# Kernel optimization log

Measured on AMD Instinct MI355X. Metric: run time of the kernel, lower is better.

Reference implementation:

```python
import jax, jax.numpy as jnp
import numpy as np

B, N, K = 1, 100000, 16
C_IN, C_OUT = 64, 128
C_MID = C_OUT // 4            # unary1 output channels (32)
PE_H = C_OUT // 4             # pe_convs hidden (32)
PE_OUT = min(C_OUT // 4, 32)  # pe_convs output (32)
WN_IN, WN_H, WN_OUT = 3, 8, 16


def _lin(key, i, o):
    return jax.random.normal(key, (i, o), jnp.float32) * (1.0 / np.sqrt(i))


def setup_inputs() -> dict:
    key = jax.random.key(0)
    ks = jax.random.split(key, 13)
    return {
        "dense_xyz": jax.random.normal(ks[0], (B, N, 3), jnp.float32),
        "dense_feats": jax.random.normal(ks[1], (B, N, C_IN), jnp.float32),
        "nei_inds": jax.random.randint(ks[2], (B, N, K), 0, N),
        "pe_w1": _lin(ks[3], 3, PE_H), "pe_b1": jnp.zeros((PE_H,), jnp.float32),
        "pe_w2": _lin(ks[4], PE_H, PE_OUT), "pe_b2": jnp.zeros((PE_OUT,), jnp.float32),
        "u1_w": _lin(ks[5], C_IN, C_MID), "u1_b": jnp.zeros((C_MID,), jnp.float32),
        "wn_w1": _lin(ks[6], WN_IN, WN_H), "wn_b1": jnp.zeros((WN_H,), jnp.float32),
        "wn_w2": _lin(ks[7], WN_H, WN_H), "wn_b2": jnp.zeros((WN_H,), jnp.float32),
        "wn_w3": _lin(ks[8], WN_H, WN_OUT), "wn_b3": jnp.zeros((WN_OUT,), jnp.float32),
        "lin_w": _lin(ks[9], (C_MID + PE_OUT) * WN_OUT, C_OUT // 2),
        "lin_b": jnp.zeros((C_OUT // 2,), jnp.float32),
        "u2_w": _lin(ks[10], C_OUT // 2, C_OUT), "u2_b": jnp.zeros((C_OUT,), jnp.float32),
        "sc_w": _lin(ks[11], C_IN, C_OUT), "sc_b": jnp.zeros((C_OUT,), jnp.float32),
    }


def _act(x):
    # act_layer = LeakyReLU(0.1)
    return jax.nn.leaky_relu(x, 0.1)


def reference(dense_xyz, dense_feats, nei_inds, pe_w1, pe_b1, pe_w2, pe_b2,
              u1_w, u1_b, wn_w1, wn_b1, wn_w2, wn_b2, wn_w3, wn_b3,
              lin_w, lin_b, u2_w, u2_b, sc_w, sc_b):
    gather = jax.vmap(lambda x, i: x[i])  # per-batch fancy gather
    g_xyz = gather(dense_xyz, nei_inds)                 # B,N,K,3
    localized = g_xyz - dense_xyz[:, :, None, :]        # weightNetInput (USE_VI=False)
    # positional-embedding WeightNet: Linear+act, Linear+act
    pe = _act(localized @ pe_w1 + pe_b1)
    pe = _act(pe @ pe_w2 + pe_b2)                       # B,N,K,PE_OUT
    # unary1 bottleneck (no act in PointLinearLayer default)
    feats = dense_feats @ u1_w + u1_b                   # B,N,C_MID
    g_feat = gather(feats, nei_inds)                    # B,N,K,C_MID
    new_feat = jnp.concatenate([g_feat, pe], axis=-1)   # B,N,K,C_MID+PE_OUT
    # WeightNet on localized coords: act, none, act
    w = _act(localized @ wn_w1 + wn_b1)
    w = w @ wn_w2 + wn_b2
    w = _act(w @ wn_w3 + wn_b3)                         # B,N,K,WN_OUT
    # PointConv aggregation: feats^T @ weights over neighbors
    agg = jnp.einsum('bnkc,bnkw->bncw', new_feat, w)
    agg = agg.reshape(agg.shape[0], agg.shape[1], -1)   # B,N,(C_MID+PE_OUT)*WN_OUT
    x = _act(agg @ lin_w + lin_b)                       # linear + act (norm=None)
    x = x @ u2_w + u2_b                                 # unary2, no act
    shortcut = dense_feats @ sc_w + sc_b                # unary_shortcut (in!=out)
    out = _act(x + shortcut)
    return out, localized
```

## Files before the change

### kernel.cpp

```cpp
#include <hip/hip_runtime.h>
#include <stdint.h>

#define NPTS 100000
#define KNEI 16
#define CIN 64
#define CMID 32
#define CONC 64
#define LINI 1024
#define COUT 128
#define APITCH 1032

typedef unsigned short u16;
typedef unsigned int u32;
typedef __attribute__((ext_vector_type(8))) short bf16x8;
typedef __attribute__((ext_vector_type(4))) float f32x4;

#define WS_PACKB  6400000
#define WS_PACKW2 (WS_PACKB + 131072)
#define WS_WN     (WS_PACKW2 + 32768)

#define NB_U1 1563
#define NB_PACK 256
#define NB_PACKW2 64

__device__ __forceinline__ float lrelu(float x) { return x > 0.f ? x : 0.1f * x; }

__device__ __forceinline__ u32 f2bf(float f) {
    union { float f; u32 u; } v; v.f = f;
    return (v.u + 0x7FFFu + ((v.u >> 16) & 1u)) >> 16;
}
__device__ __forceinline__ u16 f2bfF(float f) {
    union { float f; u32 u; } v; v.f = f;
    return (u16)((v.u + 0x8000u) >> 16);
}
__device__ __forceinline__ u32 pkbf(float a, float b) {
    union { float f; u32 u; } x, y; x.f = a; y.f = b;
    return __builtin_amdgcn_perm(y.u + 0x8000u, x.u + 0x8000u, 0x07060302u);
}
__device__ __forceinline__ float bf2f(u32 h) {
    union { u32 u; float f; } v; v.u = h << 16; return v.f;
}

__global__ __launch_bounds__(256) void k_prep(
    const float* __restrict__ df, const float* __restrict__ u1_w,
    const float* __restrict__ u1_b, u32* __restrict__ feats2,
    const float* __restrict__ lin_w, u16* __restrict__ packB,
    const float* __restrict__ u2_w, const float* __restrict__ sc_w,
    u16* __restrict__ packW2,
    const float* __restrict__ wn_w2, const float* __restrict__ wn_b2,
    const float* __restrict__ wn_w3, const float* __restrict__ wn_b3,
    float* __restrict__ wnf)
{
    int bid = blockIdx.x;
    if (bid < NB_U1) {
        const int wv = threadIdx.x >> 6, lane = threadIdx.x & 63;
        const int quad = lane >> 4, nl = lane & 15;
        const int pbase = bid * 64 + wv * 16;
        if (pbase >= NPTS) return;

        bf16x8 bw[2][2];
        #pragma unroll
        for (int nt = 0; nt < 2; ++nt)
            #pragma unroll
            for (int kk = 0; kk < 2; ++kk)
                #pragma unroll
                for (int j = 0; j < 8; ++j)
                    bw[nt][kk][j] = (short)f2bf(u1_w[(kk * 32 + quad * 8 + j) * CMID + nt * 16 + nl]);

        const float* arow = df + (size_t)(pbase + nl) * CIN + quad * 8;
        float4 a0 = *(const float4*)(arow + 0);
        float4 a1 = *(const float4*)(arow + 4);
        float4 a2 = *(const float4*)(arow + 32);
        float4 a3 = *(const float4*)(arow + 36);
        bf16x8 afr0, afr1;
        u32* ap0 = (u32*)&afr0; u32* ap1 = (u32*)&afr1;
        ap0[0] = pkbf(a0.x, a0.y); ap0[1] = pkbf(a0.z, a0.w);
        ap0[2] = pkbf(a1.x, a1.y); ap0[3] = pkbf(a1.z, a1.w);
        ap1[0] = pkbf(a2.x, a2.y); ap1[1] = pkbf(a2.z, a2.w);
        ap1[2] = pkbf(a3.x, a3.y); ap1[3] = pkbf(a3.z, a3.w);

        const f32x4 z = {0.f, 0.f, 0.f, 0.f};
        f32x4 acc0 = z, acc1 = z;
        acc0 = __builtin_amdgcn_mfma_f32_16x16x32_bf16(afr0, bw[0][0], acc0, 0, 0, 0);
        acc0 = __builtin_amdgcn_mfma_f32_16x16x32_bf16(afr1, bw[0][1], acc0, 0, 0, 0);
        acc1 = __builtin_amdgcn_mfma_f32_16x16x32_bf16(afr0, bw[1][0], acc1, 0, 0, 0);
        acc1 = __builtin_amdgcn_mfma_f32_16x16x32_bf16(afr1, bw[1][1], acc1, 0, 0, 0);

        float blo = u1_b[nl], bhi = u1_b[16 + nl];
        #pragma unroll
        for (int r = 0; r < 4; ++r) {
            int pt = pbase + quad * 4 + r;
            feats2[(size_t)pt * 16 + nl] = f2bf(acc0[r] + blo) | (f2bf(acc1[r] + bhi) << 16);
        }
    } else if (bid < NB_U1 + NB_PACK) {
        int t = (bid - NB_U1) * 256 + threadIdx.x;
        int j = t & 7, ln = (t >> 3) & 63, s = t >> 9;
        int nt = s & 3, kb = s >> 2;
        int k = kb * 32 + (ln >> 4) * 8 + j;
        int n = nt * 16 + (ln & 15);
        packB[t] = (u16)f2bf(lin_w[k * 64 + n]);
    } else if (bid < NB_U1 + NB_PACK + NB_PACKW2) {
        int t = (bid - NB_U1 - NB_PACK) * 256 + threadIdx.x;
        int j = t & 7, ln = (t >> 3) & 63, s = t >> 9;
        int nt2 = s & 7, kb2 = s >> 3;
        int k = kb2 * 32 + (ln >> 4) * 8 + j;
        int n = nt2 * 16 + (ln & 15);
        float v = (k < 64) ? u2_w[k * COUT + n] : sc_w[(k - 64) * COUT + n];
        packW2[t] = (u16)f2bf(v);
    } else {
        int t = threadIdx.x;
        if (t < 128) {
            int i = t >> 4, o = t & 15;
            float a = 0.f;
            #pragma unroll
            for (int m = 0; m < 8; ++m) a += wn_w2[i * 8 + m] * wn_w3[m * 16 + o];
            wnf[i * 16 + o] = a;
        } else if (t < 144) {
            int o = t - 128;
            float a = wn_b3[o];
            #pragma unroll
            for (int m = 0; m < 8; ++m) a += wn_b2[m] * wn_w3[m * 16 + o];
            wnf[128 + o] = a;
        }
    }
}

__global__ __launch_bounds__(256) void k_fused(
    const float* __restrict__ xyz, const int* __restrict__ nei,
    const u32* __restrict__ feats2,
    const float* __restrict__ pe_w1, const float* __restrict__ pe_b1,
    const float* __restrict__ pe_w2, const float* __restrict__ pe_b2,
    const float* __restrict__ wn_w1, const float* __restrict__ wn_b1,
    const float* __restrict__ wnf,
    const u16* __restrict__ packB, const u16* __restrict__ packW2,
    const float* __restrict__ lin_b,
    const float* __restrict__ u2_b, const float* __restrict__ sc_b,
    const float* __restrict__ df, float* __restrict__ out,
    float* __restrict__ locout)
{
    __shared__ __align__(16) u16 aggL[16 * APITCH];
    __shared__ float loc_s[4][4][16][3];
    __shared__ int   idx_s[4][4][16];
    __shared__ __align__(16) u16 pexd[4][32][24];
    __shared__ __align__(16) u16 w_s[4][16][24];
    __shared__ __align__(16) u16 h1_s[4][4][16][8];

    u16* xd = &pexd[0][0][0];

    const int tid = threadIdx.x, wv = tid >> 6, lane = tid & 63;
    const int quad = lane >> 4, nl = lane & 15;
    const int p0 = blockIdx.x * 16;
    const int ptBase = p0 + wv * 4;

    int pt0 = ptBase + quad;
    int idx0 = nei[pt0 * KNEI + nl];
    idx_s[wv][quad][nl] = idx0;
    {
        float cx = xyz[pt0 * 3 + 0], cy = xyz[pt0 * 3 + 1], cz = xyz[pt0 * 3 + 2];
        float lx0 = xyz[idx0 * 3 + 0] - cx;
        float ly0 = xyz[idx0 * 3 + 1] - cy;
        float lz0 = xyz[idx0 * 3 + 2] - cz;
        loc_s[wv][quad][nl][0] = lx0;
        loc_s[wv][quad][nl][1] = ly0;
        loc_s[wv][quad][nl][2] = lz0;
        float* lo = locout + (size_t)(pt0 * KNEI + nl) * 3;
        lo[0] = lx0; lo[1] = ly0; lo[2] = lz0;
        uint4 hp;
        u32* hpp = (u32*)&hp;
        #pragma unroll
        for (int h = 0; h < 8; h += 2) {
            float a = lrelu(wn_b1[h]     + lx0 * wn_w1[h]     + ly0 * wn_w1[8 + h]     + lz0 * wn_w1[16 + h]);
            float b = lrelu(wn_b1[h + 1] + lx0 * wn_w1[h + 1] + ly0 * wn_w1[8 + h + 1] + lz0 * wn_w1[16 + h + 1]);
            hpp[h >> 1] = pkbf(a, b);
        }
        *(uint4*)&h1_s[wv][quad][nl][0] = hp;
    }

    float w1r0[8], w1r1[8], w1r2[8], b1v[8];
    #pragma unroll
    for (int j = 0; j < 8; ++j) {
        int h = quad * 8 + j;
        w1r0[j] = pe_w1[h]; w1r1[j] = pe_w1[32 + h]; w1r2[j] = pe_w1[64 + h];
        b1v[j] = pe_b1[h];
    }
    bf16x8 w2t[2];
    #pragma unroll
    for (int ct = 0; ct < 2; ++ct)
        #pragma unroll
        for (int j = 0; j < 8; ++j)
            w2t[ct][j] = (short)f2bf(pe_w2[(quad * 8 + j) * 32 + nl + 16 * ct]);
    float b2v[2][4];
    #pragma unroll
    for (int ct = 0; ct < 2; ++ct)
        #pragma unroll
        for (int r = 0; r < 4; ++r)
            b2v[ct][r] = pe_b2[16 * ct + quad * 4 + r];
    float wn3v[8][4], b23v[4];
    #pragma unroll
    for (int h = 0; h < 8; ++h)
        #pragma unroll
        for (int r = 0; r < 4; ++r)
            wn3v[h][r] = wnf[h * 16 + quad * 4 + r];
    #pragma unroll
    for (int r = 0; r < 4; ++r) b23v[r] = wnf[128 + quad * 4 + r];

    const f32x4 zacc = {0.f, 0.f, 0.f, 0.f};

    for (int p = 0; p < 4; ++p) {
        const int m = wv * 4 + p;

        bf16x8 featf0 = 0, featf1 = 0;
        if (quad < 2) {
            #pragma unroll
            for (int j = 0; j < 8; ++j) {
                int idk = idx_s[wv][p][quad * 8 + j];
                u32 v = feats2[(size_t)idk * 16 + nl];
                featf0[j] = (short)(v & 0xffffu);
                featf1[j] = (short)(v >> 16);
            }
        }

        float lx = loc_s[wv][p][nl][0];
        float ly = loc_s[wv][p][nl][1];
        float lz = loc_s[wv][p][nl][2];

        bf16x8 phf;
        {
            u32* ph32 = (u32*)&phf;
            #pragma unroll
            for (int j = 0; j < 8; j += 2) {
                float v0 = lrelu(b1v[j]     + lx * w1r0[j]     + ly * w1r1[j]     + lz * w1r2[j]);
                float v1 = lrelu(b1v[j + 1] + lx * w1r0[j + 1] + ly * w1r1[j + 1] + lz * w1r2[j + 1]);
                ph32[j >> 1] = pkbf(v0, v1);
            }
        }

        f32x4 pe0 = __builtin_amdgcn_mfma_f32_16x16x32_bf16(w2t[0], phf, zacc, 0, 0, 0);
        f32x4 pe1 = __builtin_amdgcn_mfma_f32_16x16x32_bf16(w2t[1], phf, zacc, 0, 0, 0);

        #pragma unroll
        for (int r = 0; r < 4; ++r) {
            pexd[wv][quad * 4 + r][nl]      = f2bfF(lrelu(pe0[r] + b2v[0][r]));
            pexd[wv][16 + quad * 4 + r][nl] = f2bfF(lrelu(pe1[r] + b2v[1][r]));
        }

        {
            uint4 hv = *(const uint4*)&h1_s[wv][p][nl][0];
            float h1f[8];
            h1f[0] = bf2f(hv.x & 0xffffu); h1f[1] = bf2f(hv.x >> 16);
            h1f[2] = bf2f(hv.y & 0xffffu); h1f[3] = bf2f(hv.y >> 16);
            h1f[4] = bf2f(hv.z & 0xffffu); h1f[5] = bf2f(hv.z >> 16);
            h1f[6] = bf2f(hv.w & 0xffffu); h1f[7] = bf2f(hv.w >> 16);
            #pragma unroll
            for (int r = 0; r < 4; ++r) {
                float a = b23v[r];
                #pragma unroll
                for (int h = 0; h < 8; ++h) a += h1f[h] * wn3v[h][r];
                w_s[wv][quad * 4 + r][nl] = f2bfF(lrelu(a));
            }
        }

        bf16x8 wA = 0, peB0 = 0, peB1 = 0;
        if (quad < 2) {
            wA   = *(const bf16x8*)&w_s[wv][nl][quad * 8];
            peB0 = *(const bf16x8*)&pexd[wv][nl][quad * 8];
            peB1 = *(const bf16x8*)&pexd[wv][nl + 16][quad * 8];
        }

        f32x4 c0a = __builtin_amdgcn_mfma_f32_16x16x32_bf16(wA, featf0, zacc, 0, 0, 0);
        f32x4 c1a = __builtin_amdgcn_mfma_f32_16x16x32_bf16(wA, featf1, zacc, 0, 0, 0);
        f32x4 c2a = __builtin_amdgcn_mfma_f32_16x16x32_bf16(wA, peB0, zacc, 0, 0, 0);
        f32x4 c3a = __builtin_amdgcn_mfma_f32_16x16x32_bf16(wA, peB1, zacc, 0, 0, 0);

        {
            u16* arow = aggL + m * APITCH;
            f32x4 cc[4] = {c0a, c1a, c2a, c3a};
            #pragma unroll
            for (int ct = 0; ct < 4; ++ct) {
                int e = (nl + 16 * ct) * 16 + quad * 4;
                uint2 o;
                o.x = pkbf(cc[ct][0], cc[ct][1]);
                o.y = pkbf(cc[ct][2], cc[ct][3]);
                *(uint2*)(arow + e) = o;
            }
        }
    }
    __syncthreads();

    const int nt = wv;
    {
        const u16* bp = packB + nt * 512 + lane * 8;
        const u16* arow = aggL + nl * APITCH;
        f32x4 accA = zacc, accB = zacc;
        #pragma unroll
        for (int kk = 0; kk < 16; ++kk) {
            int kbA = 2 * kk, kbB = 2 * kk + 1;
            bf16x8 aA = *(const bf16x8*)(arow + (4 * kbA + quad) * 8);
            bf16x8 aB = *(const bf16x8*)(arow + (4 * kbB + quad) * 8);
            bf16x8 bA = *(const bf16x8*)(bp + kbA * 2048);
            bf16x8 bB = *(const bf16x8*)(bp + kbB * 2048);
            accA = __builtin_amdgcn_mfma_f32_16x16x32_bf16(aA, bA, accA, 0, 0, 0);
            accB = __builtin_amdgcn_mfma_f32_16x16x32_bf16(aB, bB, accB, 0, 0, 0);
        }
        int col = nt * 16 + nl;
        float lb = lin_b[col];
        int kb2 = col >> 5, q2 = (col >> 3) & 3, j2 = col & 7;
        #pragma unroll
        for (int r = 0; r < 4; ++r) {
            int mm = quad * 4 + r;
            float v = lrelu(accA[r] + accB[r] + lb);
            xd[(kb2 * 64 + q2 * 16 + mm) * 8 + j2] = f2bfF(v);
        }
    }
    if (tid < 128) {
        int mm = tid >> 3, cg = tid & 7;
        int colk = 64 + cg * 8;
        const float* dfr = df + (size_t)(p0 + mm) * CIN + cg * 8;
        float4 f0 = *(const float4*)(dfr);
        float4 f1 = *(const float4*)(dfr + 4);
        int kb2 = colk >> 5, q2 = (colk >> 3) & 3;
        uint4 o;
        o.x = pkbf(f0.x, f0.y);
        o.y = pkbf(f0.z, f0.w);
        o.z = pkbf(f1.x, f1.y);
        o.w = pkbf(f1.z, f1.w);
        *(uint4*)(xd + (kb2 * 64 + q2 * 16 + mm) * 8) = o;
    }
    __syncthreads();

    {
        f32x4 acc20 = zacc, acc21 = zacc;
        #pragma unroll
        for (int kb = 0; kb < 4; ++kb) {
            bf16x8 a = *(const bf16x8*)(xd + (kb * 64 + lane) * 8);
            bf16x8 b0 = *(const bf16x8*)(packW2 + (size_t)(kb * 8 + wv * 2 + 0) * 512 + lane * 8);
            bf16x8 b1 = *(const bf16x8*)(packW2 + (size_t)(kb * 8 + wv * 2 + 1) * 512 + lane * 8);
            acc20 = __builtin_amdgcn_mfma_f32_16x16x32_bf16(a, b0, acc20, 0, 0, 0);
            acc21 = __builtin_amdgcn_mfma_f32_16x16x32_bf16(a, b1, acc21, 0, 0, 0);
        }
        #pragma unroll
        for (int t = 0; t < 2; ++t) {
            f32x4 ac = t ? acc21 : acc20;
            int colo = (wv * 2 + t) * 16 + nl;
            float bias = u2_b[colo] + sc_b[colo];
            #pragma unroll
            for (int r = 0; r < 4; ++r) {
                int mm = quad * 4 + r;
                out[(size_t)(p0 + mm) * COUT + colo] = lrelu(ac[r] + bias);
            }
        }
    }
}

extern "C" void kernel_launch(void* const* d_in, const int* in_sizes, int n_in,
                              void* d_out, int out_size, void* d_ws, size_t ws_size,
                              hipStream_t stream) {
    const float* xyz   = (const float*)d_in[0];
    const float* df    = (const float*)d_in[1];
    const int*   nei   = (const int*)d_in[2];
    const float* pe_w1 = (const float*)d_in[3];
    const float* pe_b1 = (const float*)d_in[4];
    const float* pe_w2 = (const float*)d_in[5];
    const float* pe_b2 = (const float*)d_in[6];
    const float* u1_w  = (const float*)d_in[7];
    const float* u1_b  = (const float*)d_in[8];
    const float* wn_w1 = (const float*)d_in[9];
    const float* wn_b1 = (const float*)d_in[10];
    const float* wn_w2 = (const float*)d_in[11];
    const float* wn_b2 = (const float*)d_in[12];
    const float* wn_w3 = (const float*)d_in[13];
    const float* wn_b3 = (const float*)d_in[14];
    const float* lin_w = (const float*)d_in[15];
    const float* lin_b = (const float*)d_in[16];
    const float* u2_w  = (const float*)d_in[17];
    const float* u2_b  = (const float*)d_in[18];
    const float* sc_w  = (const float*)d_in[19];
    const float* sc_b  = (const float*)d_in[20];

    u32* feats2 = (u32*)d_ws;
    u16* packB  = (u16*)((char*)d_ws + WS_PACKB);
    u16* packW2 = (u16*)((char*)d_ws + WS_PACKW2);
    float* wnf  = (float*)((char*)d_ws + WS_WN);
    float* outp = (float*)d_out;
    float* locout = outp + (size_t)NPTS * COUT;

    hipLaunchKernelGGL(k_prep, dim3(NB_U1 + NB_PACK + NB_PACKW2 + 1), dim3(256), 0, stream,
                       df, u1_w, u1_b, feats2, lin_w, packB, u2_w, sc_w, packW2,
                       wn_w2, wn_b2, wn_w3, wn_b3, wnf);

    hipLaunchKernelGGL(k_fused, dim3(NPTS / 16), dim3(256), 0, stream,
                       xyz, nei, feats2,
                       pe_w1, pe_b1, pe_w2, pe_b2,
                       wn_w1, wn_b1, wnf,
                       packB, packW2, lin_b, u2_b, sc_b,
                       df, outp, locout);
}
```

Measured before the change: 227.2 us.

## Process two point groups per block and amortize weight setup in prep and fused kernels

The fused kernel now loops over two 16-point groups per block and launches half as many blocks, so per-thread register loads of the small MLP weights are paid once per 32 points. The prep kernel likewise lets each wave handle four 16-point tiles, so the bf16 u1 weight fragments are built once per 64 points instead of once per 16. Smaller tweaks replace the branchy leaky ReLU with fmaxf, unpack gathered features with byte-permute instructions, and write the localized output as a float3 store. The cost is fewer blocks in flight, which can hide less latency, plus an extra block-wide barrier between the two groups.

```diff
diff --git a/kernel.cpp b/kernel.cpp
--- a/kernel.cpp
+++ b/kernel.cpp
@@ -19,11 +19,11 @@
 #define WS_PACKW2 (WS_PACKB + 131072)
 #define WS_WN     (WS_PACKW2 + 32768)
 
-#define NB_U1 1563
+#define NB_U1 391
 #define NB_PACK 256
 #define NB_PACKW2 64
 
-__device__ __forceinline__ float lrelu(float x) { return x > 0.f ? x : 0.1f * x; }
+__device__ __forceinline__ float lrelu(float x) { return fmaxf(x, 0.1f * x); }
 
 __device__ __forceinline__ u32 f2bf(float f) {
     union { float f; u32 u; } v; v.f = f;
@@ -55,8 +55,8 @@
     if (bid < NB_U1) {
         const int wv = threadIdx.x >> 6, lane = threadIdx.x & 63;
         const int quad = lane >> 4, nl = lane & 15;
-        const int pbase = bid * 64 + wv * 16;
-        if (pbase >= NPTS) return;
+        const int base = bid * 256 + wv * 64;
+        if (base >= NPTS) return;
 
         bf16x8 bw[2][2];
         #pragma unroll
@@ -67,30 +67,37 @@
                 for (int j = 0; j < 8; ++j)
                     bw[nt][kk][j] = (short)f2bf(u1_w[(kk * 32 + quad * 8 + j) * CMID + nt * 16 + nl]);
 
-        const float* arow = df + (size_t)(pbase + nl) * CIN + quad * 8;
-        float4 a0 = *(const float4*)(arow + 0);
-        float4 a1 = *(const float4*)(arow + 4);
-        float4 a2 = *(const float4*)(arow + 32);
-        float4 a3 = *(const float4*)(arow + 36);
-        bf16x8 afr0, afr1;
-        u32* ap0 = (u32*)&afr0; u32* ap1 = (u32*)&afr1;
-        ap0[0] = pkbf(a0.x, a0.y); ap0[1] = pkbf(a0.z, a0.w);
-        ap0[2] = pkbf(a1.x, a1.y); ap0[3] = pkbf(a1.z, a1.w);
-        ap1[0] = pkbf(a2.x, a2.y); ap1[1] = pkbf(a2.z, a2.w);
-        ap1[2] = pkbf(a3.x, a3.y); ap1[3] = pkbf(a3.z, a3.w);
-
+        float blo = u1_b[nl], bhi = u1_b[16 + nl];
         const f32x4 z = {0.f, 0.f, 0.f, 0.f};
-        f32x4 acc0 = z, acc1 = z;
-        acc0 = __builtin_amdgcn_mfma_f32_16x16x32_bf16(afr0, bw[0][0], acc0, 0, 0, 0);
-        acc0 = __builtin_amdgcn_mfma_f32_16x16x32_bf16(afr1, bw[0][1], acc0, 0, 0, 0);
-        acc1 = __builtin_amdgcn_mfma_f32_16x16x32_bf16(afr0, bw[1][0], acc1, 0, 0, 0);
-        acc1 = __builtin_amdgcn_mfma_f32_16x16x32_bf16(afr1, bw[1][1], acc1, 0, 0, 0);
-
-        float blo = u1_b[nl], bhi = u1_b[16 + nl];
+
         #pragma unroll
-        for (int r = 0; r < 4; ++r) {
-            int pt = pbase + quad * 4 + r;
-            feats2[(size_t)pt * 16 + nl] = f2bf(acc0[r] + blo) | (f2bf(acc1[r] + bhi) << 16);
+        for (int g = 0; g < 4; ++g) {
+            int pbase = base + g * 16;
+            if (pbase >= NPTS) break;
+
+            const float* arow = df + (size_t)(pbase + nl) * CIN + quad * 8;
+            float4 a0 = *(const float4*)(arow + 0);
+            float4 a1 = *(const float4*)(arow + 4);
+            float4 a2 = *(const float4*)(arow + 32);
+            float4 a3 = *(const float4*)(arow + 36);
+            bf16x8 afr0, afr1;
+            u32* ap0 = (u32*)&afr0; u32* ap1 = (u32*)&afr1;
+            ap0[0] = pkbf(a0.x, a0.y); ap0[1] = pkbf(a0.z, a0.w);
+            ap0[2] = pkbf(a1.x, a1.y); ap0[3] = pkbf(a1.z, a1.w);
+            ap1[0] = pkbf(a2.x, a2.y); ap1[1] = pkbf(a2.z, a2.w);
+            ap1[2] = pkbf(a3.x, a3.y); ap1[3] = pkbf(a3.z, a3.w);
+
+            f32x4 acc0 = z, acc1 = z;
+            acc0 = __builtin_amdgcn_mfma_f32_16x16x32_bf16(afr0, bw[0][0], acc0, 0, 0, 0);
+            acc0 = __builtin_amdgcn_mfma_f32_16x16x32_bf16(afr1, bw[0][1], acc0, 0, 0, 0);
+            acc1 = __builtin_amdgcn_mfma_f32_16x16x32_bf16(afr0, bw[1][0], acc1, 0, 0, 0);
+            acc1 = __builtin_amdgcn_mfma_f32_16x16x32_bf16(afr1, bw[1][1], acc1, 0, 0, 0);
+
+            #pragma unroll
+            for (int r = 0; r < 4; ++r) {
+                int pt = pbase + quad * 4 + r;
+                feats2[(size_t)pt * 16 + nl] = f2bf(acc0[r] + blo) | (f2bf(acc1[r] + bhi) << 16);
+            }
         }
     } else if (bid < NB_U1 + NB_PACK) {
         int t = (bid - NB_U1) * 256 + threadIdx.x;
@@ -149,32 +156,6 @@
 
     const int tid = threadIdx.x, wv = tid >> 6, lane = tid & 63;
     const int quad = lane >> 4, nl = lane & 15;
-    const int p0 = blockIdx.x * 16;
-    const int ptBase = p0 + wv * 4;
-
-    int pt0 = ptBase + quad;
-    int idx0 = nei[pt0 * KNEI + nl];
-    idx_s[wv][quad][nl] = idx0;
-    {
-        float cx = xyz[pt0 * 3 + 0], cy = xyz[pt0 * 3 + 1], cz = xyz[pt0 * 3 + 2];
-        float lx0 = xyz[idx0 * 3 + 0] - cx;
-        float ly0 = xyz[idx0 * 3 + 1] - cy;
-        float lz0 = xyz[idx0 * 3 + 2] - cz;
-        loc_s[wv][quad][nl][0] = lx0;
-        loc_s[wv][quad][nl][1] = ly0;
-        loc_s[wv][quad][nl][2] = lz0;
-        float* lo = locout + (size_t)(pt0 * KNEI + nl) * 3;
-        lo[0] = lx0; lo[1] = ly0; lo[2] = lz0;
-        uint4 hp;
-        u32* hpp = (u32*)&hp;
-        #pragma unroll
-        for (int h = 0; h < 8; h += 2) {
-            float a = lrelu(wn_b1[h]     + lx0 * wn_w1[h]     + ly0 * wn_w1[8 + h]     + lz0 * wn_w1[16 + h]);
-            float b = lrelu(wn_b1[h + 1] + lx0 * wn_w1[h + 1] + ly0 * wn_w1[8 + h + 1] + lz0 * wn_w1[16 + h + 1]);
-            hpp[h >> 1] = pkbf(a, b);
-        }
-        *(uint4*)&h1_s[wv][quad][nl][0] = hp;
-    }
 
     float w1r0[8], w1r1[8], w1r2[8], b1v[8];
     #pragma unroll
@@ -206,147 +187,183 @@
 
     const f32x4 zacc = {0.f, 0.f, 0.f, 0.f};
 
-    for (int p = 0; p < 4; ++p) {
-        const int m = wv * 4 + p;
-
-        bf16x8 featf0 = 0, featf1 = 0;
-        if (quad < 2) {
-            #pragma unroll
-            for (int j = 0; j < 8; ++j) {
-                int idk = idx_s[wv][p][quad * 8 + j];
-                u32 v = feats2[(size_t)idk * 16 + nl];
-                featf0[j] = (short)(v & 0xffffu);
-                featf1[j] = (short)(v >> 16);
-            }
-        }
-
-        float lx = loc_s[wv][p][nl][0];
-        float ly = loc_s[wv][p][nl][1];
-        float lz = loc_s[wv][p][nl][2];
-
-        bf16x8 phf;
+    for (int g = 0; g < 2; ++g) {
+        if (g) __syncthreads();
+        const int p0 = blockIdx.x * 32 + g * 16;
+
+        int pt0 = p0 + wv * 4 + quad;
+        int idx0 = nei[pt0 * KNEI + nl];
+        idx_s[wv][quad][nl] = idx0;
         {
-            u32* ph32 = (u32*)&phf;
-            #pragma unroll
-            for (int j = 0; j < 8; j += 2) {
-                float v0 = lrelu(b1v[j]     + lx * w1r0[j]     + ly * w1r1[j]     + lz * w1r2[j]);
-                float v1 = lrelu(b1v[j + 1] + lx * w1r0[j + 1] + ly * w1r1[j + 1] + lz * w1r2[j + 1]);
-                ph32[j >> 1] = pkbf(v0, v1);
-            }
-        }
-
-        f32x4 pe0 = __builtin_amdgcn_mfma_f32_16x16x32_bf16(w2t[0], phf, zacc, 0, 0, 0);
-        f32x4 pe1 = __builtin_amdgcn_mfma_f32_16x16x32_bf16(w2t[1], phf, zacc, 0, 0, 0);
-
-        #pragma unroll
-        for (int r = 0; r < 4; ++r) {
-            pexd[wv][quad * 4 + r][nl]      = f2bfF(lrelu(pe0[r] + b2v[0][r]));
-            pexd[wv][16 + quad * 4 + r][nl] = f2bfF(lrelu(pe1[r] + b2v[1][r]));
-        }
-
+            float cx = xyz[pt0 * 3 + 0], cy = xyz[pt0 * 3 + 1], cz = xyz[pt0 * 3 + 2];
+            float lx0 = xyz[idx0 * 3 + 0] - cx;
+            float ly0 = xyz[idx0 * 3 + 1] - cy;
+            float lz0 = xyz[idx0 * 3 + 2] - cz;
+            loc_s[wv][quad][nl][0] = lx0;
+            loc_s[wv][quad][nl][1] = ly0;
+            loc_s[wv][quad][nl][2] = lz0;
+            float3 lv; lv.x = lx0; lv.y = ly0; lv.z = lz0;
+            *(float3*)(locout + (size_t)(pt0 * KNEI + nl) * 3) = lv;
+            uint4 hp;
+            u32* hpp = (u32*)&hp;
+            #pragma unroll
+            for (int h = 0; h < 8; h += 2) {
+                float a = lrelu(wn_b1[h]     + lx0 * wn_w1[h]     + ly0 * wn_w1[8 + h]     + lz0 * wn_w1[16 + h]);
+                float b = lrelu(wn_b1[h + 1] + lx0 * wn_w1[h + 1] + ly0 * wn_w1[8 + h + 1] + lz0 * wn_w1[16 + h + 1]);
+                hpp[h >> 1] = pkbf(a, b);
+            }
+            *(uint4*)&h1_s[wv][quad][nl][0] = hp;
+        }
+
+        for (int p = 0; p < 4; ++p) {
+            const int m = wv * 4 + p;
+
+            bf16x8 featf0 = 0, featf1 = 0;
+            if (quad < 2) {
+                u32 gv[8];
+                #pragma unroll
+                for (int j = 0; j < 8; ++j) {
+                    int idk = idx_s[wv][p][quad * 8 + j];
+                    gv[j] = feats2[(size_t)idk * 16 + nl];
+                }
+                u32* f0w = (u32*)&featf0;
+                u32* f1w = (u32*)&featf1;
+                #pragma unroll
+                for (int jp = 0; jp < 4; ++jp) {
+                    u32 a = gv[2 * jp], b = gv[2 * jp + 1];
+                    f0w[jp] = __builtin_amdgcn_perm(b, a, 0x05040100u);
+                    f1w[jp] = __builtin_amdgcn_perm(b, a, 0x07060302u);
+                }
+            }
+
+            float lx = loc_s[wv][p][nl][0];
+            float ly = loc_s[wv][p][nl][1];
+            float lz = loc_s[wv][p][nl][2];
+
+            bf16x8 phf;
+            {
+                u32* ph32 = (u32*)&phf;
+                #pragma unroll
+                for (int j = 0; j < 8; j += 2) {
+                    float v0 = lrelu(b1v[j]     + lx * w1r0[j]     + ly * w1r1[j]     + lz * w1r2[j]);
+                    float v1 = lrelu(b1v[j + 1] + lx * w1r0[j + 1] + ly * w1r1[j + 1] + lz * w1r2[j + 1]);
+                    ph32[j >> 1] = pkbf(v0, v1);
+                }
+            }
+
+            f32x4 pe0 = __builtin_amdgcn_mfma_f32_16x16x32_bf16(w2t[0], phf, zacc, 0, 0, 0);
+            f32x4 pe1 = __builtin_amdgcn_mfma_f32_16x16x32_bf16(w2t[1], phf, zacc, 0, 0, 0);
+
+            #pragma unroll
+            for (int r = 0; r < 4; ++r) {
+                pexd[wv][quad * 4 + r][nl]      = f2bfF(lrelu(pe0[r] + b2v[0][r]));
+                pexd[wv][16 + quad * 4 + r][nl] = f2bfF(lrelu(pe1[r] + b2v[1][r]));
+            }
+
+            {
+                uint4 hv = *(const uint4*)&h1_s[wv][p][nl][0];
+                float h1f[8];
+                h1f[0] = bf2f(hv.x & 0xffffu); h1f[1] = bf2f(hv.x >> 16);
+                h1f[2] = bf2f(hv.y & 0xffffu); h1f[3] = bf2f(hv.y >> 16);
+                h1f[4] = bf2f(hv.z & 0xffffu); h1f[5] = bf2f(hv.z >> 16);
+                h1f[6] = bf2f(hv.w & 0xffffu); h1f[7] = bf2f(hv.w >> 16);
+                #pragma unroll
+                for (int r = 0; r < 4; ++r) {
+                    float a = b23v[r];
+                    #pragma unroll
+                    for (int h = 0; h < 8; ++h) a += h1f[h] * wn3v[h][r];
+                    w_s[wv][quad * 4 + r][nl] = f2bfF(lrelu(a));
+                }
+            }
+
+            bf16x8 wA = 0, peB0 = 0, peB1 = 0;
+            if (quad < 2) {
+                wA   = *(const bf16x8*)&w_s[wv][nl][quad * 8];
+                peB0 = *(const bf16x8*)&pexd[wv][nl][quad * 8];
+                peB1 = *(const bf16x8*)&pexd[wv][nl + 16][quad * 8];
+            }
+
+            f32x4 c0a = __builtin_amdgcn_mfma_f32_16x16x32_bf16(wA, featf0, zacc, 0, 0, 0);
+            f32x4 c1a = __builtin_amdgcn_mfma_f32_16x16x32_bf16(wA, featf1, zacc, 0, 0, 0);
+            f32x4 c2a = __builtin_amdgcn_mfma_f32_16x16x32_bf16(wA, peB0, zacc, 0, 0, 0);
+            f32x4 c3a = __builtin_amdgcn_mfma_f32_16x16x32_bf16(wA, peB1, zacc, 0, 0, 0);
+
+            {
+                u16* arow = aggL + m * APITCH;
+                f32x4 cc[4] = {c0a, c1a, c2a, c3a};
+                #pragma unroll
+                for (int ct = 0; ct < 4; ++ct) {
+                    int e = (nl + 16 * ct) * 16 + quad * 4;
+                    uint2 o;
+                    o.x = pkbf(cc[ct][0], cc[ct][1]);
+                    o.y = pkbf(cc[ct][2], cc[ct][3]);
+                    *(uint2*)(arow + e) = o;
+                }
+            }
+        }
+        __syncthreads();
+
+        const int nt = wv;
         {
-            uint4 hv = *(const uint4*)&h1_s[wv][p][nl][0];
-            float h1f[8];
-            h1f[0] = bf2f(hv.x & 0xffffu); h1f[1] = bf2f(hv.x >> 16);
-            h1f[2] = bf2f(hv.y & 0xffffu); h1f[3] = bf2f(hv.y >> 16);
-            h1f[4] = bf2f(hv.z & 0xffffu); h1f[5] = bf2f(hv.z >> 16);
-            h1f[6] = bf2f(hv.w & 0xffffu); h1f[7] = bf2f(hv.w >> 16);
-            #pragma unroll
-            for (int r = 0; r < 4; ++r) {
-                float a = b23v[r];
-                #pragma unroll
-                for (int h = 0; h < 8; ++h) a += h1f[h] * wn3v[h][r];
-                w_s[wv][quad * 4 + r][nl] = f2bfF(lrelu(a));
-            }
-        }
-
-        bf16x8 wA = 0, peB0 = 0, peB1 = 0;
-        if (quad < 2) {
-            wA   = *(const bf16x8*)&w_s[wv][nl][quad * 8];
-            peB0 = *(const bf16x8*)&pexd[wv][nl][quad * 8];
-            peB1 = *(const bf16x8*)&pexd[wv][nl + 16][quad * 8];
-        }
-
-        f32x4 c0a = __builtin_amdgcn_mfma_f32_16x16x32_bf16(wA, featf0, zacc, 0, 0, 0);
-        f32x4 c1a = __builtin_amdgcn_mfma_f32_16x16x32_bf16(wA, featf1, zacc, 0, 0, 0);
-        f32x4 c2a = __builtin_amdgcn_mfma_f32_16x16x32_bf16(wA, peB0, zacc, 0, 0, 0);
-        f32x4 c3a = __builtin_amdgcn_mfma_f32_16x16x32_bf16(wA, peB1, zacc, 0, 0, 0);
-
-        {
-            u16* arow = aggL + m * APITCH;
-            f32x4 cc[4] = {c0a, c1a, c2a, c3a};
-            #pragma unroll
-            for (int ct = 0; ct < 4; ++ct) {
-                int e = (nl + 16 * ct) * 16 + quad * 4;
-                uint2 o;
-                o.x = pkbf(cc[ct][0], cc[ct][1]);
-                o.y = pkbf(cc[ct][2], cc[ct][3]);
-                *(uint2*)(arow + e) = o;
-            }
-        }
-    }
-    __syncthreads();
-
-    const int nt = wv;
-    {
-        const u16* bp = packB + nt * 512 + lane * 8;
-        const u16* arow = aggL + nl * APITCH;
-        f32x4 accA = zacc, accB = zacc;
-        #pragma unroll
-        for (int kk = 0; kk < 16; ++kk) {
-            int kbA = 2 * kk, kbB = 2 * kk + 1;
-            bf16x8 aA = *(const bf16x8*)(arow + (4 * kbA + quad) * 8);
-            bf16x8 aB = *(const bf16x8*)(arow + (4 * kbB + quad) * 8);
-            bf16x8 bA = *(const bf16x8*)(bp + kbA * 2048);
-            bf16x8 bB = *(const bf16x8*)(bp + kbB * 2048);
-            accA = __builtin_amdgcn_mfma_f32_16x16x32_bf16(aA, bA, accA, 0, 0, 0);
-            accB = __builtin_amdgcn_mfma_f32_16x16x32_bf16(aB, bB, accB, 0, 0, 0);
-        }
-        int col = nt * 16 + nl;
-        float lb = lin_b[col];
-        int kb2 = col >> 5, q2 = (col >> 3) & 3, j2 = col & 7;
-        #pragma unroll
-        for (int r = 0; r < 4; ++r) {
-            int mm = quad * 4 + r;
-            float v = lrelu(accA[r] + accB[r] + lb);
-            xd[(kb2 * 64 + q2 * 16 + mm) * 8 + j2] = f2bfF(v);
-        }
-    }
-    if (tid < 128) {
-        int mm = tid >> 3, cg = tid & 7;
-        int colk = 64 + cg * 8;
-        const float* dfr = df + (size_t)(p0 + mm) * CIN + cg * 8;
-        float4 f0 = *(const float4*)(dfr);
-        float4 f1 = *(const float4*)(dfr + 4);
-        int kb2 = colk >> 5, q2 = (colk >> 3) & 3;
-        uint4 o;
-        o.x = pkbf(f0.x, f0.y);
-        o.y = pkbf(f0.z, f0.w);
-        o.z = pkbf(f1.x, f1.y);
-        o.w = pkbf(f1.z, f1.w);
-        *(uint4*)(xd + (kb2 * 64 + q2 * 16 + mm) * 8) = o;
-    }
-    __syncthreads();
-
-    {
-        f32x4 acc20 = zacc, acc21 = zacc;
-        #pragma unroll
-        for (int kb = 0; kb < 4; ++kb) {
-            bf16x8 a = *(const bf16x8*)(xd + (kb * 64 + lane) * 8);
-            bf16x8 b0 = *(const bf16x8*)(packW2 + (size_t)(kb * 8 + wv * 2 + 0) * 512 + lane * 8);
-            bf16x8 b1 = *(const bf16x8*)(packW2 + (size_t)(kb * 8 + wv * 2 + 1) * 512 + lane * 8);
-            acc20 = __builtin_amdgcn_mfma_f32_16x16x32_bf16(a, b0, acc20, 0, 0, 0);
-            acc21 = __builtin_amdgcn_mfma_f32_16x16x32_bf16(a, b1, acc21, 0, 0, 0);
-        }
-        #pragma unroll
-        for (int t = 0; t < 2; ++t) {
-            f32x4 ac = t ? acc21 : acc20;
-            int colo = (wv * 2 + t) * 16 + nl;
-            float bias = u2_b[colo] + sc_b[colo];
+            const u16* bp = packB + nt * 512 + lane * 8;
+            const u16* arow = aggL + nl * APITCH;
+            f32x4 accA = zacc, accB = zacc;
+            #pragma unroll
+            for (int kk = 0; kk < 16; ++kk) {
+                int kbA = 2 * kk, kbB = 2 * kk + 1;
+                bf16x8 aA = *(const bf16x8*)(arow + (4 * kbA + quad) * 8);
+                bf16x8 aB = *(const bf16x8*)(arow + (4 * kbB + quad) * 8);
+                bf16x8 bA = *(const bf16x8*)(bp + kbA * 2048);
+                bf16x8 bB = *(const bf16x8*)(bp + kbB * 2048);
+                accA = __builtin_amdgcn_mfma_f32_16x16x32_bf16(aA, bA, accA, 0, 0, 0);
+                accB = __builtin_amdgcn_mfma_f32_16x16x32_bf16(aB, bB, accB, 0, 0, 0);
+            }
+            int col = nt * 16 + nl;
+            float lb = lin_b[col];
+            int kb2 = col >> 5, q2 = (col >> 3) & 3, j2 = col & 7;
             #pragma unroll
             for (int r = 0; r < 4; ++r) {
                 int mm = quad * 4 + r;
-                out[(size_t)(p0 + mm) * COUT + colo] = lrelu(ac[r] + bias);
+                float v = lrelu(accA[r] + accB[r] + lb);
+                xd[(kb2 * 64 + q2 * 16 + mm) * 8 + j2] = f2bfF(v);
+            }
+        }
+        if (tid < 128) {
+            int mm = tid >> 3, cg = tid & 7;
+            int colk = 64 + cg * 8;
+            const float* dfr = df + (size_t)(p0 + mm) * CIN + cg * 8;
+            float4 f0 = *(const float4*)(dfr);
+            float4 f1 = *(const float4*)(dfr + 4);
+            int kb2 = colk >> 5, q2 = (colk >> 3) & 3;
+            uint4 o;
+            o.x = pkbf(f0.x, f0.y);
+            o.y = pkbf(f0.z, f0.w);
+            o.z = pkbf(f1.x, f1.y);
+            o.w = pkbf(f1.z, f1.w);
+            *(uint4*)(xd + (kb2 * 64 + q2 * 16 + mm) * 8) = o;
+        }
+        __syncthreads();
+
+        {
+            f32x4 acc20 = zacc, acc21 = zacc;
+            #pragma unroll
+            for (int kb = 0; kb < 4; ++kb) {
+                bf16x8 a = *(const bf16x8*)(xd + (kb * 64 + lane) * 8);
+                bf16x8 b0 = *(const bf16x8*)(packW2 + (size_t)(kb * 8 + wv * 2 + 0) * 512 + lane * 8);
+                bf16x8 b1 = *(const bf16x8*)(packW2 + (size_t)(kb * 8 + wv * 2 + 1) * 512 + lane * 8);
+                acc20 = __builtin_amdgcn_mfma_f32_16x16x32_bf16(a, b0, acc20, 0, 0, 0);
+                acc21 = __builtin_amdgcn_mfma_f32_16x16x32_bf16(a, b1, acc21, 0, 0, 0);
+            }
+            #pragma unroll
+            for (int t = 0; t < 2; ++t) {
+                f32x4 ac = t ? acc21 : acc20;
+                int colo = (wv * 2 + t) * 16 + nl;
+                float bias = u2_b[colo] + sc_b[colo];
+                #pragma unroll
+                for (int r = 0; r < 4; ++r) {
+                    int mm = quad * 4 + r;
+                    out[(size_t)(p0 + mm) * COUT + colo] = lrelu(ac[r] + bias);
+                }
             }
         }
     }
@@ -388,7 +405,7 @@
                        df, u1_w, u1_b, feats2, lin_w, packB, u2_w, sc_w, packW2,
                        wn_w2, wn_b2, wn_w3, wn_b3, wnf);
 
-    hipLaunchKernelGGL(k_fused, dim3(NPTS / 16), dim3(256), 0, stream,
+    hipLaunchKernelGGL(k_fused, dim3(NPTS / 32), dim3(256), 0, stream,
                        xyz, nei, feats2,
                        pe_w1, pe_b1, pe_w2, pe_b2,
                        wn_w1, wn_b1, wnf,
```

New measurement: 324.3 us. 1.43x slower.
